# Performance work log

Hardware: AMD Instinct MI355X
Metric: run time of the kernel (lower is better)

The kernel has to match this reference:

```python
import jax, jax.numpy as jnp
import numpy as np
from jax import lax

T, H, I, E = 1024, 1024, 512, 16          # tokens, hidden, moe_intermediate, n_routed_experts
TOP_K, N_GROUP, TOPK_GROUP = 4, 4, 2
N_SHARED = 2
I_SHARED = I * N_SHARED                    # shared-expert intermediate size
ROUTED_SCALE = 2.5


def setup_inputs() -> dict:
    key = jax.random.key(0)
    ks = jax.random.split(key, 9)
    s = lambda k, shape, fan: jax.random.normal(k, shape, jnp.float32) * (fan ** -0.5)
    return {
        "hidden_states": jax.random.normal(ks[0], (T, H), jnp.float32),
        "router_w": s(ks[1], (H, E), H),                 # gate: ReplicatedLinear(H, E)
        "e_bias": jax.random.normal(ks[2], (E,), jnp.float32) * 0.01,  # e_score_correction_bias
        "w_gate": s(ks[3], (E, H, I), H),                # routed experts gate_proj
        "w_up": s(ks[4], (E, H, I), H),                  # routed experts up_proj
        "w_down": s(ks[5], (E, I, H), I),                # routed experts down_proj
        "sw_gate": s(ks[6], (H, I_SHARED), H),           # shared experts gate_proj
        "sw_up": s(ks[7], (H, I_SHARED), H),             # shared experts up_proj
        "sw_down": s(ks[8], (I_SHARED, H), I_SHARED),    # shared experts down_proj
    }


def _grouped_topk_sigmoid(logits, e_bias):
    # DeepSeek-V3 'noaux_tc' grouped top-k with sigmoid scoring.
    scores = jax.nn.sigmoid(logits)                      # [T, E]
    sc = scores + e_bias                                 # biased scores for selection only
    g = sc.reshape(-1, N_GROUP, E // N_GROUP)
    group_scores = lax.top_k(g, 2)[0].sum(-1)            # [T, n_group]: sum of top-2 per group
    _, gidx = lax.top_k(group_scores, TOPK_GROUP)        # [T, topk_group]
    gmask = jax.nn.one_hot(gidx, N_GROUP, dtype=sc.dtype).sum(1)  # [T, n_group]
    emask = jnp.repeat(gmask, E // N_GROUP, axis=1)      # [T, E]
    masked = jnp.where(emask > 0, sc, 0.0)               # sigmoid scores are >=0
    _, tidx = lax.top_k(masked, TOP_K)                   # [T, top_k]
    w = jnp.take_along_axis(scores, tidx, axis=1)        # weights use UNbiased scores
    w = w / (w.sum(-1, keepdims=True) + 1e-20)           # norm_topk_prob=True
    # dense combine weights [T, E]
    combine = (jax.nn.one_hot(tidx, E, dtype=w.dtype) * w[..., None]).sum(1)
    return combine


def reference(hidden_states, router_w, e_bias, w_gate, w_up, w_down,
              sw_gate, sw_up, sw_down):
    x = hidden_states                                    # [T, H]
    logits = x @ router_w                                # [T, E]
    combine = _grouped_topk_sigmoid(logits, e_bias)      # [T, E]

    # routed experts: SiLU-gated MLP per expert, dense-over-experts reference
    gp = jnp.einsum('th,ehi->tei', x, w_gate)            # [T, E, I]
    up = jnp.einsum('th,ehi->tei', x, w_up)
    h = jax.nn.silu(gp) * up
    oe = jnp.einsum('tei,eih->teh', h, w_down)           # [T, E, H]
    routed = jnp.einsum('teh,te->th', oe, combine)       # [T, H]

    # shared experts MLP (reduce_results=False path), fp32 path scales routed only
    shared = (jax.nn.silu(x @ sw_gate) * (x @ sw_up)) @ sw_down  # [T, H]
    return routed * ROUTED_SCALE + shared
```

## Files before the change

### kernel.cpp

```cpp
#include <hip/hip_runtime.h>
#include <stdint.h>

#define T_TOK 1024
#define HDIM  1024
#define IDIM  512
#define NEXP  16
#define ISH   1024
#define MAXT128  48
#define HSLOTS   6144

typedef _Float16 f16;
typedef __attribute__((ext_vector_type(8))) _Float16 f16x8;
typedef __attribute__((ext_vector_type(4))) _Float16 f16x4;
typedef __attribute__((ext_vector_type(4))) float    f32x4;

__device__ __forceinline__ void gld16(const void* g, void* l) {
  __builtin_amdgcn_global_load_lds(
      (__attribute__((address_space(1))) void*)(uintptr_t)g,
      (__attribute__((address_space(3))) void*)(uint32_t)(uintptr_t)l,
      16, 0, 0);
}

__device__ __forceinline__ f16x8 ldsfragA(const f16* buf, int row, int lch) {
  int phys = lch ^ (row & 7);
  return *(const f16x8*)(buf + row * 64 + phys * 8);
}

__device__ __forceinline__ f16x8 ldsfragB(const f16* buf, int n, int kc) {
  int c = kc ^ ((n >> 3) & 7);
  return *(const f16x8*)(buf + n * 72 + c * 8);
}

__device__ __forceinline__ void stageB(const float* __restrict__ W, int ldW,
                                       int kt, int n0, f16* __restrict__ Bs,
                                       int nbase, int tid) {
  int p = tid & 31, kg = tid >> 5;
  int n = 2 * p;
  const float* src = W + (size_t)(kt + 8 * kg) * ldW + n0 + n;
  float2 v[8];
#pragma unroll
  for (int r = 0; r < 8; r++) v[r] = *(const float2*)(src + (size_t)r * ldW);
  f16x8 c0, c1;
#pragma unroll
  for (int r = 0; r < 8; r++) { c0[r] = (f16)v[r].x; c1[r] = (f16)v[r].y; }
  int nn = nbase + n;
  int cc = kg ^ ((nn >> 3) & 7);
  *(f16x8*)(Bs + (size_t)nn * 72 + cc * 8) = c0;
  *(f16x8*)(Bs + (size_t)(nn + 1) * 72 + cc * 8) = c1;
}

__global__ __launch_bounds__(256) void router_kernel(
    const float* __restrict__ x, const float* __restrict__ rw, const float* __restrict__ ebias,
    f16* __restrict__ xh, int* __restrict__ topk_i, float* __restrict__ topk_w) {
  int wave = threadIdx.x >> 6, l = threadIdx.x & 63;
  int t = blockIdx.x * 4 + wave;
  float acc[16];
#pragma unroll
  for (int e = 0; e < 16; e++) acc[e] = 0.f;
#pragma unroll
  for (int i = 0; i < 4; i++) {
    int k = i * 256 + l * 4;
    float4 xv = *(const float4*)(x + (size_t)t * HDIM + k);
    f16x4 h = { (f16)xv.x, (f16)xv.y, (f16)xv.z, (f16)xv.w };
    *(f16x4*)(xh + (size_t)t * HDIM + k) = h;
    const float* xp = &xv.x;
#pragma unroll
    for (int j = 0; j < 4; j++) {
      float xj = xp[j];
      const float4* w4 = (const float4*)(rw + (size_t)(k + j) * 16);
#pragma unroll
      for (int q = 0; q < 4; q++) {
        float4 w = w4[q];
        acc[q*4+0] += xj * w.x; acc[q*4+1] += xj * w.y;
        acc[q*4+2] += xj * w.z; acc[q*4+3] += xj * w.w;
      }
    }
  }
#pragma unroll
  for (int off = 32; off >= 1; off >>= 1)
#pragma unroll
    for (int e = 0; e < 16; e++) acc[e] += __shfl_xor(acc[e], off, 64);

  if (l == 0) {
    float s[16], sc[16];
#pragma unroll
    for (int e = 0; e < 16; e++) {
      s[e] = 1.f / (1.f + __expf(-acc[e]));
      sc[e] = s[e] + ebias[e];
    }
    float gs[4];
#pragma unroll
    for (int g = 0; g < 4; g++) {
      float a = -1e30f, b2 = -1e30f;
#pragma unroll
      for (int j = 0; j < 4; j++) {
        float v = sc[g*4 + j];
        if (v > a) { b2 = a; a = v; } else if (v > b2) { b2 = v; }
      }
      gs[g] = a + b2;
    }
    int g1 = 0;
    for (int g = 1; g < 4; g++) if (gs[g] > gs[g1]) g1 = g;
    int g2 = -1;
    for (int g = 0; g < 4; g++) if (g != g1 && (g2 < 0 || gs[g] > gs[g2])) g2 = g;
    float masked[16];
#pragma unroll
    for (int e = 0; e < 16; e++) {
      int g = e >> 2;
      masked[e] = (g == g1 || g == g2) ? sc[e] : 0.0f;
    }
    int idx[4]; float wv[4]; float denom = 1e-20f;
#pragma unroll
    for (int j = 0; j < 4; j++) {
      int best = 0; float bv = masked[0];
      for (int e = 1; e < 16; e++) if (masked[e] > bv) { bv = masked[e]; best = e; }
      idx[j] = best; wv[j] = s[best]; denom += s[best];
      masked[best] = -1e30f;
    }
#pragma unroll
    for (int j = 0; j < 4; j++) {
      topk_i[t * 4 + j] = idx[j];
      topk_w[t * 4 + j] = wv[j] / denom * 2.5f;
    }
  }
}

__global__ __launch_bounds__(1024) void scatter_kernel(
    const int* __restrict__ tki,
    int* __restrict__ tok, int* __restrict__ slotmap,
    int* __restrict__ tile_e, int* __restrict__ tile_srow,
    int* __restrict__ tile_hb, int* __restrict__ ntl) {
  __shared__ int lcnt[NEXP], lpos[NEXP], lbase[NEXP];
  int t = threadIdx.x;
  if (t < NEXP) { lcnt[t] = 0; lpos[t] = 0; }
  __syncthreads();
  int idx[4];
#pragma unroll
  for (int j = 0; j < 4; j++) idx[j] = tki[t*4+j];
#pragma unroll
  for (int j = 0; j < 4; j++) atomicAdd(&lcnt[idx[j]], 1);
  __syncthreads();
  if (t == 0) {
    int total = 0, slots = 0;
    for (int e = 0; e < NEXP; e++) {
      int c = lcnt[e], nt = (c + 127) >> 7;
      lbase[e] = slots;
      for (int j = 0; j < nt; j++) {
        tile_e[total] = e; tile_srow[total] = j * 128; tile_hb[total] = slots + j * 128; total++;
      }
      slots += nt * 128;
    }
    ntl[0] = total;
  }
  __syncthreads();
#pragma unroll
  for (int j = 0; j < 4; j++) {
    int slot = atomicAdd(&lpos[idx[j]], 1);
    tok[idx[j] * T_TOK + slot] = t;
    slotmap[t * 4 + j] = lbase[idx[j]] + slot;
  }
  __syncthreads();
  int e = t >> 6, s = t & 63;
  int c = lcnt[e];
  int top = ((c + 127) >> 7) << 7;
  for (int s2 = c + s; s2 < top; s2 += 64) tok[e * T_TOK + s2] = 0;
}

__device__ __forceinline__ f32x4 mfma16(f16x8 a, f16x8 b, f32x4 c) {
  return __builtin_amdgcn_mfma_f32_16x16x32_f16(a, b, c, 0, 0, 0);
}

__global__ __launch_bounds__(256) void gu_all(
    const f16* __restrict__ xh,
    const float* __restrict__ sg, const float* __restrict__ su, f16* __restrict__ hsh,
    const float* __restrict__ wg, const float* __restrict__ wu, f16* __restrict__ hbuf,
    const int* __restrict__ tile_e, const int* __restrict__ tile_srow,
    const int* __restrict__ tile_hb, const int* __restrict__ ntl,
    const int* __restrict__ tok) {
  int b = blockIdx.x;
  const float *Bg, *Bu; f16* Hdst;
  int e = 0, srow = 0, mbase, n0, N;
  bool gather = (b >= 128);
  if (!gather) {
    Bg = sg; Bu = su; Hdst = hsh; N = ISH;
    mbase = (b >> 4) * 128; n0 = (b & 15) * 64;
  } else {
    int rb = b - 128, by = rb >> 3;
    if (by >= ntl[0]) return;
    e = tile_e[by]; srow = tile_srow[by]; mbase = tile_hb[by];
    size_t bo = (size_t)e * HDIM * IDIM;
    Bg = wg + bo; Bu = wu + bo; Hdst = hbuf; N = IDIM;
    n0 = (rb & 7) * 64;
  }
  const int K = HDIM;

  __shared__ f16 As[128 * 64];
  __shared__ f16 Bgs[64 * 72], Bus[64 * 72];

  int tid = threadIdx.x, lane = tid & 63, wave = tid >> 6;
  int quad = lane >> 4, l15 = lane & 15;
  int r = lane >> 3, p = lane & 7;

  const f16* gbA[4]; f16* lbA[4];
#pragma unroll
  for (int jj = 0; jj < 4; jj++) {
    int j = wave * 4 + jj;
    int kcol = (p ^ r) << 3;
    int row = j * 8 + r;
    int grow = gather ? tok[e * T_TOK + srow + row] : (mbase + row);
    gbA[jj] = xh + (size_t)grow * K + kcol;
    lbA[jj] = (f16*)As + (j << 9);
  }

  int wr = wave >> 1, wc = wave & 1;
  f32x4 zero = {0.f, 0.f, 0.f, 0.f};
  f32x4 aG[4][2], aU[4][2];
#pragma unroll
  for (int mi = 0; mi < 4; mi++)
#pragma unroll
    for (int ni = 0; ni < 2; ni++) { aG[mi][ni] = zero; aU[mi][ni] = zero; }

  for (int kt = 0; kt < K; kt += 64) {
    __syncthreads();
#pragma unroll
    for (int jj = 0; jj < 4; jj++) gld16(gbA[jj] + kt, lbA[jj]);
    stageB(Bg, N, kt, n0, Bgs, 0, tid);
    stageB(Bu, N, kt, n0, Bus, 0, tid);
    __syncthreads();
#pragma unroll
    for (int ks = 0; ks < 2; ks++) {
      int lch = (ks << 2) + quad;
      f16x8 a[4], g[2], u[2];
#pragma unroll
      for (int mi = 0; mi < 4; mi++) a[mi] = ldsfragA(As, 64 * wr + 16 * mi + l15, lch);
#pragma unroll
      for (int ni = 0; ni < 2; ni++) {
        g[ni] = ldsfragB(Bgs, 32 * wc + 16 * ni + l15, lch);
        u[ni] = ldsfragB(Bus, 32 * wc + 16 * ni + l15, lch);
      }
#pragma unroll
      for (int mi = 0; mi < 4; mi++)
#pragma unroll
        for (int ni = 0; ni < 2; ni++) {
          aG[mi][ni] = mfma16(a[mi], g[ni], aG[mi][ni]);
          aU[mi][ni] = mfma16(a[mi], u[ni], aU[mi][ni]);
        }
    }
  }
#pragma unroll
  for (int mi = 0; mi < 4; mi++)
#pragma unroll
    for (int ni = 0; ni < 2; ni++)
#pragma unroll
      for (int rg = 0; rg < 4; rg++) {
        int m = 64 * wr + 16 * mi + (quad << 2) + rg;
        int n = n0 + 32 * wc + 16 * ni + l15;
        float g = aG[mi][ni][rg], u = aU[mi][ni][rg];
        float val = (g / (1.f + __expf(-g))) * u;
        Hdst[(size_t)(mbase + m) * N + n] = (f16)val;
      }
}

__global__ __launch_bounds__(256) void down_all(
    const f16* __restrict__ hsh, const float* __restrict__ sd,
    const f16* __restrict__ hbuf, const float* __restrict__ wd,
    float* __restrict__ out, f16* __restrict__ odown,
    const int* __restrict__ tile_hb, const int* __restrict__ tile_e,
    const int* __restrict__ ntl) {
  int b = blockIdx.x;
  bool routed = (b >= 64);
  const f16* A; const float* B; int K, abase, n0;
  if (!routed) {
    A = hsh; B = sd; K = ISH;
    abase = (b >> 3) * 128; n0 = (b & 7) * 128;
  } else {
    int rb = b - 64, by = rb >> 3;
    if (by >= ntl[0]) return;
    abase = tile_hb[by];
    A = hbuf; B = wd + (size_t)tile_e[by] * IDIM * HDIM; K = IDIM;
    n0 = (rb & 7) * 128;
  }

  __shared__ f16 As[128 * 64];
  __shared__ f16 Bs[128 * 72];

  int tid = threadIdx.x, lane = tid & 63, wave = tid >> 6;
  int quad = lane >> 4, l15 = lane & 15;
  int r = lane >> 3, p = lane & 7;

  const f16* gbA[4]; f16* lbA[4];
#pragma unroll
  for (int jj = 0; jj < 4; jj++) {
    int j = wave * 4 + jj;
    int kcol = (p ^ r) << 3;
    int row = j * 8 + r;
    gbA[jj] = A + (size_t)(abase + row) * K + kcol;
    lbA[jj] = (f16*)As + (j << 9);
  }

  int wr = wave >> 1, wc = wave & 1;
  f32x4 zero = {0.f, 0.f, 0.f, 0.f};
  f32x4 ac[4][4];
#pragma unroll
  for (int mi = 0; mi < 4; mi++)
#pragma unroll
    for (int ni = 0; ni < 4; ni++) ac[mi][ni] = zero;

  for (int kt = 0; kt < K; kt += 64) {
    __syncthreads();
#pragma unroll
    for (int jj = 0; jj < 4; jj++) gld16(gbA[jj] + kt, lbA[jj]);
    stageB(B, HDIM, kt, n0,      Bs, 0,  tid);
    stageB(B, HDIM, kt, n0 + 64, Bs, 64, tid);
    __syncthreads();
#pragma unroll
    for (int ks = 0; ks < 2; ks++) {
      int lch = (ks << 2) + quad;
      f16x8 a[4], bb[4];
#pragma unroll
      for (int mi = 0; mi < 4; mi++) a[mi] = ldsfragA(As, 64 * wr + 16 * mi + l15, lch);
#pragma unroll
      for (int ni = 0; ni < 4; ni++) bb[ni] = ldsfragB(Bs, 64 * wc + 16 * ni + l15, lch);
#pragma unroll
      for (int mi = 0; mi < 4; mi++)
#pragma unroll
        for (int ni = 0; ni < 4; ni++)
          ac[mi][ni] = mfma16(a[mi], bb[ni], ac[mi][ni]);
    }
  }
#pragma unroll
  for (int mi = 0; mi < 4; mi++)
#pragma unroll
    for (int ni = 0; ni < 4; ni++)
#pragma unroll
      for (int rg = 0; rg < 4; rg++) {
        int m = 64 * wr + 16 * mi + (quad << 2) + rg;
        int n = n0 + 64 * wc + 16 * ni + l15;
        if (routed) odown[(size_t)(abase + m) * HDIM + n] = (f16)ac[mi][ni][rg];
        else        out  [(size_t)(abase + m) * HDIM + n] = ac[mi][ni][rg];
      }
}

__global__ __launch_bounds__(256) void combine_kernel(
    const f16* __restrict__ odown, const int* __restrict__ slotmap,
    const float* __restrict__ tkw, float* __restrict__ out) {
  int t = blockIdx.x;
  __shared__ int ss[4]; __shared__ float sw[4];
  if (threadIdx.x < 4) {
    ss[threadIdx.x] = slotmap[t * 4 + threadIdx.x];
    sw[threadIdx.x] = tkw[t * 4 + threadIdx.x];
  }
  __syncthreads();
  int h = threadIdx.x * 4;
  float4 acc = *(const float4*)(out + (size_t)t * HDIM + h);
#pragma unroll
  for (int j = 0; j < 4; j++) {
    f16x4 v = *(const f16x4*)(odown + (size_t)ss[j] * HDIM + h);
    float wj = sw[j];
    acc.x += wj * (float)v[0]; acc.y += wj * (float)v[1];
    acc.z += wj * (float)v[2]; acc.w += wj * (float)v[3];
  }
  *(float4*)(out + (size_t)t * HDIM + h) = acc;
}

extern "C" void kernel_launch(void* const* d_in, const int* in_sizes, int n_in,
                              void* d_out, int out_size, void* d_ws, size_t ws_size,
                              hipStream_t stream) {
  const float* x  = (const float*)d_in[0];
  const float* rw = (const float*)d_in[1];
  const float* eb = (const float*)d_in[2];
  const float* wg = (const float*)d_in[3];
  const float* wu = (const float*)d_in[4];
  const float* wd = (const float*)d_in[5];
  const float* sg = (const float*)d_in[6];
  const float* su = (const float*)d_in[7];
  const float* sd = (const float*)d_in[8];
  float* out = (float*)d_out;
  (void)in_sizes; (void)n_in; (void)out_size; (void)ws_size;

  char* w = (char*)d_ws;
  size_t off = 0;
  auto alloc = [&](size_t b) { void* p = w + off; off = (off + b + 255) & ~(size_t)255; return p; };

  f16* xh   = (f16*)alloc((size_t)T_TOK * HDIM * 2);
  f16* hbuf = (f16*)alloc((size_t)HSLOTS * IDIM * 2);
  f16* hsh  = (f16*)alloc((size_t)T_TOK * ISH * 2);
  f16* odown = (f16*)alloc((size_t)HSLOTS * HDIM * 2);
  int* topk_i = (int*)alloc((size_t)T_TOK * 4 * 4);
  float* topk_w = (float*)alloc((size_t)T_TOK * 4 * 4);
  int* tok  = (int*)alloc((size_t)NEXP * T_TOK * 4);
  int* slotmap = (int*)alloc((size_t)T_TOK * 4 * 4);
  int* tile_e    = (int*)alloc(MAXT128 * 4);
  int* tile_srow = (int*)alloc(MAXT128 * 4);
  int* tile_hb   = (int*)alloc(MAXT128 * 4);
  int* ntl       = (int*)alloc(16);

  router_kernel<<<T_TOK / 4, 256, 0, stream>>>(x, rw, eb, xh, topk_i, topk_w);
  scatter_kernel<<<1, 1024, 0, stream>>>(topk_i, tok, slotmap,
                                         tile_e, tile_srow, tile_hb, ntl);
  gu_all<<<128 + MAXT128 * 8, 256, 0, stream>>>(
      xh, sg, su, hsh, wg, wu, hbuf, tile_e, tile_srow, tile_hb, ntl, tok);
  down_all<<<64 + MAXT128 * 8, 256, 0, stream>>>(
      hsh, sd, hbuf, wd, out, odown, tile_hb, tile_e, ntl);
  combine_kernel<<<T_TOK, 256, 0, stream>>>(odown, slotmap, topk_w, out);
}
```

Baseline: 226.8 us.

## Double-buffer LDS tiles and use 512-thread blocks in expert GEMMs

Both expert GEMM kernels (gate/up and down) now double-buffer their LDS tiles. The next K-tile's A rows are issued with global_load_lds and its fp32 B weights are loaded into registers while the current tile is multiplied, so only one barrier per iteration remains. Blocks grow to 512 threads (8 waves), and each wave now owns a 32-row slice instead of 64, which halves accumulator registers per wave. The cost is twice the shared memory per block, which may limit occupancy.

```diff
diff --git a/kernel.cpp b/kernel.cpp
--- a/kernel.cpp
+++ b/kernel.cpp
@@ -31,19 +31,20 @@
   return *(const f16x8*)(buf + n * 72 + c * 8);
 }
 
-__device__ __forceinline__ void stageB(const float* __restrict__ W, int ldW,
-                                       int kt, int n0, f16* __restrict__ Bs,
-                                       int nbase, int tid) {
-  int p = tid & 31, kg = tid >> 5;
-  int n = 2 * p;
-  const float* src = W + (size_t)(kt + 8 * kg) * ldW + n0 + n;
-  float2 v[8];
+__device__ __forceinline__ void loadB(const float* __restrict__ W, int ldW,
+                                      int kt, int n0, int tid2, float2* v) {
+  int p = tid2 & 31, kg = tid2 >> 5;
+  const float* src = W + (size_t)(kt + 8 * kg) * ldW + n0 + 2 * p;
 #pragma unroll
   for (int r = 0; r < 8; r++) v[r] = *(const float2*)(src + (size_t)r * ldW);
+}
+__device__ __forceinline__ void writeB(f16* __restrict__ Bs, int nbase, int tid2,
+                                       const float2* v) {
+  int p = tid2 & 31, kg = tid2 >> 5;
   f16x8 c0, c1;
 #pragma unroll
   for (int r = 0; r < 8; r++) { c0[r] = (f16)v[r].x; c1[r] = (f16)v[r].y; }
-  int nn = nbase + n;
+  int nn = nbase + 2 * p;
   int cc = kg ^ ((nn >> 3) & 7);
   *(f16x8*)(Bs + (size_t)nn * 72 + cc * 8) = c0;
   *(f16x8*)(Bs + (size_t)(nn + 1) * 72 + cc * 8) = c1;
@@ -170,7 +171,7 @@
   return __builtin_amdgcn_mfma_f32_16x16x32_f16(a, b, c, 0, 0, 0);
 }
 
-__global__ __launch_bounds__(256) void gu_all(
+__global__ __launch_bounds__(512, 4) void gu_all(
     const f16* __restrict__ xh,
     const float* __restrict__ sg, const float* __restrict__ su, f16* __restrict__ hsh,
     const float* __restrict__ wg, const float* __restrict__ wu, f16* __restrict__ hbuf,
@@ -194,17 +195,17 @@
   }
   const int K = HDIM;
 
-  __shared__ f16 As[128 * 64];
-  __shared__ f16 Bgs[64 * 72], Bus[64 * 72];
+  __shared__ f16 As[2 * 128 * 64];
+  __shared__ f16 Bgs[2 * 64 * 72], Bus[2 * 64 * 72];
 
   int tid = threadIdx.x, lane = tid & 63, wave = tid >> 6;
   int quad = lane >> 4, l15 = lane & 15;
   int r = lane >> 3, p = lane & 7;
 
-  const f16* gbA[4]; f16* lbA[4];
-#pragma unroll
-  for (int jj = 0; jj < 4; jj++) {
-    int j = wave * 4 + jj;
+  const f16* gbA[2]; f16* lbA[2];
+#pragma unroll
+  for (int jj = 0; jj < 2; jj++) {
+    int j = wave * 2 + jj;
     int kcol = (p ^ r) << 3;
     int row = j * 8 + r;
     int grow = gather ? tok[e * T_TOK + srow + row] : (mbase + row);
@@ -212,48 +213,67 @@
     lbA[jj] = (f16*)As + (j << 9);
   }
 
+  const float* Bmine = (tid < 256) ? Bg : Bu;
+  f16* Bsmine = (tid < 256) ? (f16*)Bgs : (f16*)Bus;
+  int tid2 = tid & 255;
+
   int wr = wave >> 1, wc = wave & 1;
   f32x4 zero = {0.f, 0.f, 0.f, 0.f};
-  f32x4 aG[4][2], aU[4][2];
-#pragma unroll
-  for (int mi = 0; mi < 4; mi++)
+  f32x4 aG[2][2], aU[2][2];
+#pragma unroll
+  for (int mi = 0; mi < 2; mi++)
 #pragma unroll
     for (int ni = 0; ni < 2; ni++) { aG[mi][ni] = zero; aU[mi][ni] = zero; }
 
-  for (int kt = 0; kt < K; kt += 64) {
-    __syncthreads();
-#pragma unroll
-    for (int jj = 0; jj < 4; jj++) gld16(gbA[jj] + kt, lbA[jj]);
-    stageB(Bg, N, kt, n0, Bgs, 0, tid);
-    stageB(Bu, N, kt, n0, Bus, 0, tid);
-    __syncthreads();
+  float2 v[8];
+#pragma unroll
+  for (int jj = 0; jj < 2; jj++) gld16(gbA[jj], lbA[jj]);
+  loadB(Bmine, N, 0, n0, tid2, v);
+  writeB(Bsmine, 0, tid2, v);
+  __syncthreads();
+
+  const int nk = K >> 6;
+  for (int it = 0; it < nk; ++it) {
+    int cb = it & 1, nb = cb ^ 1;
+    bool pf = (it + 1 < nk);
+    if (pf) {
+      int kt = (it + 1) << 6;
+#pragma unroll
+      for (int jj = 0; jj < 2; jj++) gld16(gbA[jj] + kt, lbA[jj] + nb * 8192);
+      loadB(Bmine, N, kt, n0, tid2, v);
+    }
+    const f16* Ab = (const f16*)As + cb * 8192;
+    const f16* Gb = (const f16*)Bgs + cb * 4608;
+    const f16* Ub = (const f16*)Bus + cb * 4608;
 #pragma unroll
     for (int ks = 0; ks < 2; ks++) {
       int lch = (ks << 2) + quad;
-      f16x8 a[4], g[2], u[2];
-#pragma unroll
-      for (int mi = 0; mi < 4; mi++) a[mi] = ldsfragA(As, 64 * wr + 16 * mi + l15, lch);
+      f16x8 a[2], g[2], u[2];
+#pragma unroll
+      for (int mi = 0; mi < 2; mi++) a[mi] = ldsfragA(Ab, 32 * wr + 16 * mi + l15, lch);
 #pragma unroll
       for (int ni = 0; ni < 2; ni++) {
-        g[ni] = ldsfragB(Bgs, 32 * wc + 16 * ni + l15, lch);
-        u[ni] = ldsfragB(Bus, 32 * wc + 16 * ni + l15, lch);
-      }
-#pragma unroll
-      for (int mi = 0; mi < 4; mi++)
+        g[ni] = ldsfragB(Gb, 32 * wc + 16 * ni + l15, lch);
+        u[ni] = ldsfragB(Ub, 32 * wc + 16 * ni + l15, lch);
+      }
+#pragma unroll
+      for (int mi = 0; mi < 2; mi++)
 #pragma unroll
         for (int ni = 0; ni < 2; ni++) {
           aG[mi][ni] = mfma16(a[mi], g[ni], aG[mi][ni]);
           aU[mi][ni] = mfma16(a[mi], u[ni], aU[mi][ni]);
         }
     }
-  }
-#pragma unroll
-  for (int mi = 0; mi < 4; mi++)
+    if (pf) writeB(Bsmine + nb * 4608, 0, tid2, v);
+    __syncthreads();
+  }
+#pragma unroll
+  for (int mi = 0; mi < 2; mi++)
 #pragma unroll
     for (int ni = 0; ni < 2; ni++)
 #pragma unroll
       for (int rg = 0; rg < 4; rg++) {
-        int m = 64 * wr + 16 * mi + (quad << 2) + rg;
+        int m = 32 * wr + 16 * mi + (quad << 2) + rg;
         int n = n0 + 32 * wc + 16 * ni + l15;
         float g = aG[mi][ni][rg], u = aU[mi][ni][rg];
         float val = (g / (1.f + __expf(-g))) * u;
@@ -261,7 +281,7 @@
       }
 }
 
-__global__ __launch_bounds__(256) void down_all(
+__global__ __launch_bounds__(512, 4) void down_all(
     const f16* __restrict__ hsh, const float* __restrict__ sd,
     const f16* __restrict__ hbuf, const float* __restrict__ wd,
     float* __restrict__ out, f16* __restrict__ odown,
@@ -281,60 +301,77 @@
     n0 = (rb & 7) * 128;
   }
 
-  __shared__ f16 As[128 * 64];
-  __shared__ f16 Bs[128 * 72];
+  __shared__ f16 As[2 * 128 * 64];
+  __shared__ f16 Bs[2 * 128 * 72];
 
   int tid = threadIdx.x, lane = tid & 63, wave = tid >> 6;
   int quad = lane >> 4, l15 = lane & 15;
   int r = lane >> 3, p = lane & 7;
 
-  const f16* gbA[4]; f16* lbA[4];
-#pragma unroll
-  for (int jj = 0; jj < 4; jj++) {
-    int j = wave * 4 + jj;
+  const f16* gbA[2]; f16* lbA[2];
+#pragma unroll
+  for (int jj = 0; jj < 2; jj++) {
+    int j = wave * 2 + jj;
     int kcol = (p ^ r) << 3;
     int row = j * 8 + r;
     gbA[jj] = A + (size_t)(abase + row) * K + kcol;
     lbA[jj] = (f16*)As + (j << 9);
   }
 
+  int nb0 = (tid < 256) ? 0 : 64;
+  int tid2 = tid & 255;
+
   int wr = wave >> 1, wc = wave & 1;
   f32x4 zero = {0.f, 0.f, 0.f, 0.f};
-  f32x4 ac[4][4];
-#pragma unroll
-  for (int mi = 0; mi < 4; mi++)
+  f32x4 ac[2][4];
+#pragma unroll
+  for (int mi = 0; mi < 2; mi++)
 #pragma unroll
     for (int ni = 0; ni < 4; ni++) ac[mi][ni] = zero;
 
-  for (int kt = 0; kt < K; kt += 64) {
-    __syncthreads();
-#pragma unroll
-    for (int jj = 0; jj < 4; jj++) gld16(gbA[jj] + kt, lbA[jj]);
-    stageB(B, HDIM, kt, n0,      Bs, 0,  tid);
-    stageB(B, HDIM, kt, n0 + 64, Bs, 64, tid);
-    __syncthreads();
+  float2 v[8];
+#pragma unroll
+  for (int jj = 0; jj < 2; jj++) gld16(gbA[jj], lbA[jj]);
+  loadB(B, HDIM, 0, n0 + nb0, tid2, v);
+  writeB((f16*)Bs, nb0, tid2, v);
+  __syncthreads();
+
+  const int nk = K >> 6;
+  for (int it = 0; it < nk; ++it) {
+    int cb = it & 1, nb = cb ^ 1;
+    bool pf = (it + 1 < nk);
+    if (pf) {
+      int kt = (it + 1) << 6;
+#pragma unroll
+      for (int jj = 0; jj < 2; jj++) gld16(gbA[jj] + kt, lbA[jj] + nb * 8192);
+      loadB(B, HDIM, kt, n0 + nb0, tid2, v);
+    }
+    const f16* Ab = (const f16*)As + cb * 8192;
+    const f16* Bb = (const f16*)Bs + cb * 9216;
 #pragma unroll
     for (int ks = 0; ks < 2; ks++) {
       int lch = (ks << 2) + quad;
-      f16x8 a[4], bb[4];
-#pragma unroll
-      for (int mi = 0; mi < 4; mi++) a[mi] = ldsfragA(As, 64 * wr + 16 * mi + l15, lch);
-#pragma unroll
-      for (int ni = 0; ni < 4; ni++) bb[ni] = ldsfragB(Bs, 64 * wc + 16 * ni + l15, lch);
-#pragma unroll
-      for (int mi = 0; mi < 4; mi++)
+      f16x8 a[2], bb[4];
+#pragma unroll
+      for (int mi = 0; mi < 2; mi++) a[mi] = ldsfragA(Ab, 32 * wr + 16 * mi + l15, lch);
+#pragma unroll
+      for (int ni = 0; ni < 4; ni++) bb[ni] = ldsfragB(Bb, 64 * wc + 16 * ni + l15, lch);
+#pragma unroll
+      for (int mi = 0; mi < 2; mi++)
 #pragma unroll
         for (int ni = 0; ni < 4; ni++)
           ac[mi][ni] = mfma16(a[mi], bb[ni], ac[mi][ni]);
     }
-  }
-#pragma unroll
-  for (int mi = 0; mi < 4; mi++)
+    if (pf) writeB((f16*)Bs + nb * 9216, nb0, tid2, v);
+    __syncthreads();
+  }
+#pragma unroll
+  for (int mi = 0; mi < 2; mi++)
 #pragma unroll
     for (int ni = 0; ni < 4; ni++)
 #pragma unroll
       for (int rg = 0; rg < 4; rg++) {
-        int m = 64 * wr + 16 * mi + (quad << 2) + rg;
+        int m = 32 * wr + 16 * mi + (quad << 2) + rg;
         int n = n0 + 64 * wc + 16 * ni + l15;
         if (routed) odown[(size_t)(abase + m) * HDIM + n] = (f16)ac[mi][ni][rg];
         else        out  [(size_t)(abase + m) * HDIM + n] = ac[mi][ni][rg];
@@ -398,9 +435,9 @@
   router_kernel<<<T_TOK / 4, 256, 0, stream>>>(x, rw, eb, xh, topk_i, topk_w);
   scatter_kernel<<<1, 1024, 0, stream>>>(topk_i, tok, slotmap,
                                          tile_e, tile_srow, tile_hb, ntl);
-  gu_all<<<128 + MAXT128 * 8, 256, 0, stream>>>(
+  gu_all<<<128 + MAXT128 * 8, 512, 0, stream>>>(
       xh, sg, su, hsh, wg, wu, hbuf, tile_e, tile_srow, tile_hb, ntl, tok);
-  down_all<<<64 + MAXT128 * 8, 256, 0, stream>>>(
+  down_all<<<64 + MAXT128 * 8, 512, 0, stream>>>(
       hsh, sd, hbuf, wd, out, odown, tile_hb, tile_e, ntl);
   combine_kernel<<<T_TOK, 256, 0, stream>>>(odown, slotmap, topk_w, out);
 }
```

After: 221.5 us. -2.3%, faster.
